# Performance work log

Hardware: AMD Instinct MI355X
Metric: run time of the kernel (lower is better)

The kernel has to match this reference:

```python
import jax, jax.numpy as jnp
import numpy as np

# Fixed problem sizes (match input_specs): B graphs of N points each, kNN with K neighbors.
B, N, K = 32, 2048, 20
F_IN, H, C = 3, 64, 40
BN = B * N
E = BN * K


def mlp(x, w1, b1, w2, b2):
    # PyG MLP([in, H, H]) with plain last layer: Lin -> ReLU -> Lin
    return jax.nn.relu(x @ w1 + b1) @ w2 + b2


def edge_conv(x, src, dst, w1, b1, w2, b2):
    # EdgeConv message for edge j->i: MLP(cat[x_i, x_j - x_i]); aggr='max' at target i.
    xi = x[dst]                      # [E, F]
    xj = x[src]                      # [E, F]
    msg = mlp(jnp.concatenate([xi, xj - xi], axis=-1), w1, b1, w2, b2)  # [E, H]
    out = jax.ops.segment_max(msg, dst, num_segments=x.shape[0])        # [BN, H]
    # nodes with no incoming edges: -inf -> 0 (torch_scatter max fill behavior)
    return jnp.where(jnp.isfinite(out), out, jnp.zeros((), out.dtype))


def dynamic_edge_conv(x, w1, b1, w2, b2):
    # Rebuild kNN graph from current features within each graph, then EdgeConv(max).
    xb = x.reshape(B, N, -1)                                   # [B, N, H]
    sq = jnp.sum(xb * xb, axis=-1)                             # [B, N]
    # squared euclidean distances [B, N, N]
    d = sq[:, :, None] - 2.0 * jnp.einsum('bnh,bmh->bnm', xb, xb) + sq[:, None, :]
    _, idx = jax.lax.top_k(-d, K)                              # [B, N, K] nearest (incl. self)
    xj = jax.vmap(lambda xg, ig: xg[ig])(xb, idx)              # [B, N, K, H]
    xi = jnp.broadcast_to(xb[:, :, None, :], xj.shape)         # [B, N, K, H]
    msg = mlp(jnp.concatenate([xi, xj - xi], axis=-1), w1, b1, w2, b2)  # [B, N, K, H]
    return jnp.max(msg, axis=2).reshape(BN, -1)                # exactly K msgs per node


def _lin_init(key, fan_in, fan_out):
    k1, k2 = jax.random.split(key)
    s = 1.0 / np.sqrt(fan_in)
    w = jax.random.uniform(k1, (fan_in, fan_out), jnp.float32, -s, s)
    b = jax.random.uniform(k2, (fan_out,), jnp.float32, -s, s)
    return w, b


def setup_inputs() -> dict:
    key = jax.random.key(0)
    ks = jax.random.split(key, 10)
    x = jax.random.normal(ks[0], (BN, F_IN), jnp.float32)
    edge_index = jax.random.randint(ks[1], (2, E), 0, BN, jnp.int64)
    batch = (jnp.arange(BN) // N).astype(jnp.int64)
    c1_w1, c1_b1 = _lin_init(ks[2], 2 * F_IN, H)
    c1_w2, c1_b2 = _lin_init(ks[3], H, H)
    d1_w1, d1_b1 = _lin_init(ks[4], 2 * H, H)
    d1_w2, d1_b2 = _lin_init(ks[5], H, H)
    d2_w1, d2_b1 = _lin_init(ks[6], 2 * H, H)
    d2_w2, d2_b2 = _lin_init(ks[7], H, H)
    lin_w, lin_b = _lin_init(ks[8], H, C)
    return dict(x=x, edge_index=edge_index, batch=batch,
                c1_w1=c1_w1, c1_b1=c1_b1, c1_w2=c1_w2, c1_b2=c1_b2,
                d1_w1=d1_w1, d1_b1=d1_b1, d1_w2=d1_w2, d1_b2=d1_b2,
                d2_w1=d2_w1, d2_b1=d2_b1, d2_w2=d2_w2, d2_b2=d2_b2,
                lin_w=lin_w, lin_b=lin_b)


def reference(x, edge_index, batch,
              c1_w1, c1_b1, c1_w2, c1_b2,
              d1_w1, d1_b1, d1_w2, d1_b2,
              d2_w1, d2_b1, d2_w2, d2_b2,
              lin_w, lin_b):
    # batch is assumed sorted with equal-size graphs (arange // N); kNN is done per graph.
    src, dst = edge_index[0], edge_index[1]
    h = edge_conv(x, src, dst, c1_w1, c1_b1, c1_w2, c1_b2)
    h = dynamic_edge_conv(jax.nn.elu(h), d1_w1, d1_b1, d1_w2, d1_b2)
    h = dynamic_edge_conv(jax.nn.elu(h), d2_w1, d2_b1, d2_w2, d2_b2)
    return h @ lin_w + lin_b
```

## Files before the change

kernel.cpp:

```cpp
#include <hip/hip_runtime.h>
#include <math.h>

#define Bg 32
#define Ng 2048
#define Kn 20
#define BNn (Bg*Ng)
#define En (BNn*Kn)
#define Hd 64
#define Cd 40

#define KK 24
#define CAPB 7

typedef __attribute__((ext_vector_type(8))) short bf16x8;
typedef __attribute__((ext_vector_type(4))) float f32x4;

__device__ __forceinline__ unsigned enc_f32(float f){
  unsigned u = __float_as_uint(f);
  return ((int)u < 0) ? ~u : (u | 0x80000000u);
}

__device__ __forceinline__ unsigned short bf16rne(float f){
  unsigned u = __float_as_uint(f);
  return (unsigned short)((u + 0x7FFFu + ((u >> 16) & 1u)) >> 16);
}

__global__ void prep_w_kernel(const float* __restrict__ w1c, const float* __restrict__ w1d1,
                              const float* __restrict__ w1d2,
                              float* __restrict__ wpq0, float* __restrict__ wpq1,
                              float* __restrict__ wpq2){
  int t = blockIdx.x*256 + threadIdx.x;
  if (t < 3*128){
    int d = t >> 7, l = t & 127;
    wpq0[t] = (l < 64) ? (w1c[d*64 + l] - w1c[(d+3)*64 + l]) : w1c[(d+3)*64 + (l-64)];
  }
  if (t < 64*128){
    int d = t >> 7, l = t & 127;
    wpq1[t] = (l < 64) ? (w1d1[d*64 + l] - w1d1[(d+64)*64 + l]) : w1d1[(d+64)*64 + (l-64)];
    wpq2[t] = (l < 64) ? (w1d2[d*64 + l] - w1d2[(d+64)*64 + l]) : w1d2[(d+64)*64 + (l-64)];
  }
}

__global__ void zero_kernel(int* __restrict__ p){
  p[blockIdx.x*256 + threadIdx.x] = 0;
}

__global__ void init_enc_kernel(unsigned int* __restrict__ enc){
  enc[blockIdx.x*256 + threadIdx.x] = 0x007FFFFFu;
}

template<int D>
__global__ __launch_bounds__(128) void gemm_pq_kernel(const float* __restrict__ x,
                               const float* __restrict__ w,
                               float* __restrict__ P, float* __restrict__ Q){
  __shared__ float xs[8*D];
  int l = threadIdx.x;
  int node0 = blockIdx.x*8;
  float wc[D];
  #pragma unroll
  for (int d=0; d<D; d++) wc[d] = w[d*128 + l];
  for (int i=l; i < 8*D; i += 128) xs[i] = x[(size_t)node0*D + i];
  __syncthreads();
  #pragma unroll
  for (int n=0; n<8; n++){
    float s = 0.f;
    #pragma unroll
    for (int d=0; d<D; d++) s = fmaf(xs[n*D+d], wc[d], s);
    int node = node0 + n;
    if (l < 64) P[(size_t)node*64 + l] = s;
    else        Q[(size_t)node*64 + (l-64)] = s;
  }
}

__global__ __launch_bounds__(256) void sqxb_kernel(const float* __restrict__ x,
        float* __restrict__ sq, unsigned short* __restrict__ xb){
  int t = blockIdx.x*256 + threadIdx.x;
  int node = t >> 6, l = t & 63;
  float v = x[t];
  xb[t] = bf16rne(v);
  float s = v*v;
  #pragma unroll
  for (int o=32; o; o>>=1) s += __shfl_xor(s, o, 64);
  if (l == 0) sq[node] = s;
}

__global__ __launch_bounds__(256) void decode_sqxb_kernel(const unsigned int* __restrict__ enc,
        const float* __restrict__ b2, float* __restrict__ x,
        float* __restrict__ sq, unsigned short* __restrict__ xb){
  int t = blockIdx.x*256 + threadIdx.x;
  int node = t >> 6, l = t & 63;
  unsigned int e = enc[t];
  unsigned int bits = (e & 0x80000000u) ? (e ^ 0x80000000u) : ~e;
  float f = __uint_as_float(bits);
  if (isfinite(f)) f += b2[l]; else f = 0.f;
  f = f > 0.f ? f : expm1f(f);
  x[t] = f;
  xb[t] = bf16rne(f);
  float s = f*f;
  #pragma unroll
  for (int o=32; o; o>>=1) s += __shfl_xor(s, o, 64);
  if (l == 0) sq[node] = s;
}

__global__ void count_kernel(const int* __restrict__ ei, int* __restrict__ deg){
  int e = blockIdx.x*256 + threadIdx.x;
  atomicAdd(&deg[ei[En + e]], 1);
}

__global__ __launch_bounds__(1024) void scan_kernel(const int* __restrict__ deg,
        int* __restrict__ rowptr, int* __restrict__ cursor){
  __shared__ int ps[1024];
  int t = threadIdx.x;
  int base = t*64;
  int s = 0;
  for (int k=0;k<64;k++) s += deg[base+k];
  ps[t] = s; __syncthreads();
  for (int off=1; off<1024; off<<=1){
    int v = (t>=off) ? ps[t-off] : 0;
    __syncthreads();
    ps[t] += v;
    __syncthreads();
  }
  int run = (t>0) ? ps[t-1] : 0;
  for (int k=0;k<64;k++){
    rowptr[base+k] = run; cursor[base+k] = run;
    run += deg[base+k];
  }
  if (t==1023) rowptr[BNn] = run;
}

__global__ void scatter_kernel(const int* __restrict__ ei, int* __restrict__ cursor,
                               int* __restrict__ csrc, int* __restrict__ enid){
  int e = blockIdx.x*256 + threadIdx.x;
  int s = ei[e], d = ei[En + e];
  int pos = atomicAdd(&cursor[d], 1);
  csrc[pos] = s;
  enid[pos] = d;
}

#define SWZ16(base, row, stridep2, byteoff) \
  ((unsigned short*)((char*)(base) + ((((row) << (stridep2)) + (byteoff)) ^ (((row) & 7) << 4))))

__global__ __launch_bounds__(256,3) void econv_gemm_kernel(
    const int* __restrict__ csrc, const int* __restrict__ enid,
    const float* __restrict__ P, const float* __restrict__ Q,
    const float* __restrict__ b1, const float* __restrict__ w2,
    unsigned int* __restrict__ enc){
  __shared__ __align__(16) char smem[49152];
  unsigned short* Ah = (unsigned short*)smem;
  unsigned short* Al = (unsigned short*)(smem + 16384);
  unsigned short* Wh = (unsigned short*)(smem + 32768);
  unsigned short* Wl = (unsigned short*)(smem + 40960);
  float* Ct = (float*)smem;
  __shared__ int eids[256];
  int tid = threadIdx.x;
  int lane = tid & 63, w = tid >> 6;
  int e0 = ((blockIdx.x & 7)*640 + (blockIdx.x >> 3))*256;

  eids[tid] = enid[e0 + tid];
  #pragma unroll
  for (int z = 0; z < 16; z++){
    int idx = z*256 + tid;
    int k = idx >> 6, n = idx & 63;
    float f = w2[idx];
    unsigned short h = bf16rne(f);
    float fh = __uint_as_float((unsigned)h << 16);
    unsigned short l = bf16rne(f - fh);
    *SWZ16(Wh, n, 7, k*2) = h;
    *SWZ16(Wl, n, 7, k*2) = l;
  }

  #pragma unroll 1
  for (int hh = 0; hh < 2; hh++){
    int eh0 = e0 + hh*128;
    __syncthreads();
    {
      int el = tid >> 1, kh2 = (tid & 1) * 32;
      int e = eh0 + el;
      int i = eids[hh*128 + el];
      int j = csrc[e];
      const float* Pr = P + (size_t)i*Hd + kh2;
      const float* Qr = Q + (size_t)j*Hd + kh2;
      const float* Br = b1 + kh2;
      #pragma unroll
      for (int m = 0; m < 4; m++){
        float4 pa = ((const float4*)Pr)[2*m], pb = ((const float4*)Pr)[2*m+1];
        float4 qa = ((const float4*)Qr)[2*m], qb = ((const float4*)Qr)[2*m+1];
        float4 ba = ((const float4*)Br)[2*m], bbv = ((const float4*)Br)[2*m+1];
        float a[8];
        a[0]=fmaxf(pa.x+qa.x+ba.x,0.f);  a[1]=fmaxf(pa.y+qa.y+ba.y,0.f);
        a[2]=fmaxf(pa.z+qa.z+ba.z,0.f);  a[3]=fmaxf(pa.w+qa.w+ba.w,0.f);
        a[4]=fmaxf(pb.x+qb.x+bbv.x,0.f); a[5]=fmaxf(pb.y+qb.y+bbv.y,0.f);
        a[6]=fmaxf(pb.z+qb.z+bbv.z,0.f); a[7]=fmaxf(pb.w+qb.w+bbv.w,0.f);
        unsigned hw[4], lw[4];
        #pragma unroll
        for (int t=0;t<4;t++){
          unsigned short h0 = bf16rne(a[2*t]);
          unsigned short h1 = bf16rne(a[2*t+1]);
          float f0 = __uint_as_float((unsigned)h0 << 16);
          float f1 = __uint_as_float((unsigned)h1 << 16);
          unsigned short l0 = bf16rne(a[2*t] - f0);
          unsigned short l1 = bf16rne(a[2*t+1] - f1);
          hw[t] = (unsigned)h0 | ((unsigned)h1 << 16);
          lw[t] = (unsigned)l0 | ((unsigned)l1 << 16);
        }
        uint4 hv = {hw[0], hw[1], hw[2], hw[3]};
        uint4 lv = {lw[0], lw[1], lw[2], lw[3]};
        *(uint4*)SWZ16(Ah, el, 7, (kh2 + 8*m)*2) = hv;
        *(uint4*)SWZ16(Al, el, 7, (kh2 + 8*m)*2) = lv;
      }
    }
    __syncthreads();
    bf16x8 Af[2][2], Lf[2][2];
    #pragma unroll
    for (int mt=0; mt<2; mt++)
      #pragma unroll
      for (int s=0; s<2; s++){
        int row = w*32 + mt*16 + (lane & 15);
        Af[mt][s] = *(const bf16x8*)SWZ16(Ah, row, 7, (s*32 + (lane>>4)*8)*2);
        Lf[mt][s] = *(const bf16x8*)SWZ16(Al, row, 7, (s*32 + (lane>>4)*8)*2);
      }
    f32x4 acc[2][4];
    #pragma unroll
    for (int mt=0; mt<2; mt++)
      #pragma unroll
      for (int nt=0; nt<4; nt++)
        acc[mt][nt] = (f32x4){0.f,0.f,0.f,0.f};
    #pragma unroll
    for (int nt=0; nt<4; nt++){
      int n = nt*16 + (lane & 15);
      bf16x8 Bh0 = *(const bf16x8*)SWZ16(Wh, n, 7, ((lane>>4)*8)*2);
      bf16x8 Bh1 = *(const bf16x8*)SWZ16(Wh, n, 7, (32 + (lane>>4)*8)*2);
      bf16x8 Bl0 = *(const bf16x8*)SWZ16(Wl, n, 7, ((lane>>4)*8)*2);
      bf16x8 Bl1 = *(const bf16x8*)SWZ16(Wl, n, 7, (32 + (lane>>4)*8)*2);
      #pragma unroll
      for (int mt=0; mt<2; mt++){
        f32x4 a_ = acc[mt][nt];
        a_ = __builtin_amdgcn_mfma_f32_16x16x32_bf16(Af[mt][0], Bh0, a_, 0, 0, 0);
        a_ = __builtin_amdgcn_mfma_f32_16x16x32_bf16(Af[mt][1], Bh1, a_, 0, 0, 0);
        a_ = __builtin_amdgcn_mfma_f32_16x16x32_bf16(Af[mt][0], Bl0, a_, 0, 0, 0);
        a_ = __builtin_amdgcn_mfma_f32_16x16x32_bf16(Af[mt][1], Bl1, a_, 0, 0, 0);
        a_ = __builtin_amdgcn_mfma_f32_16x16x32_bf16(Lf[mt][0], Bh0, a_, 0, 0, 0);
        a_ = __builtin_amdgcn_mfma_f32_16x16x32_bf16(Lf[mt][1], Bh1, a_, 0, 0, 0);
        acc[mt][nt] = a_;
      }
    }
    __syncthreads();
    #pragma unroll
    for (int mt=0; mt<2; mt++){
      int rb = w*32 + mt*16 + (lane>>4)*4;
      #pragma unroll
      for (int nt=0; nt<4; nt++){
        int ch = nt*16 + (lane & 15);
        #pragma unroll
        for (int v=0; v<4; v++)
          Ct[ch*128 + ((rb+v) ^ (ch & 31))] = acc[mt][nt][v];
      }
    }
    __syncthreads();
    {
      int ch = tid & 63, part = tid >> 6;
      int rbase = part*32;
      int cur = eids[hh*128 + rbase];
      float vmax = -INFINITY;
      #pragma unroll 1
      for (int r = 0; r < 32; r++){
        int row = rbase + r;
        int id = eids[hh*128 + row];
        float v = Ct[ch*128 + (row ^ (ch & 31))];
        if (id != cur){
          atomicMax(&enc[(size_t)cur*Hd + ch], enc_f32(vmax));
          vmax = -INFINITY; cur = id;
        }
        vmax = fmaxf(vmax, v);
      }
      atomicMax(&enc[(size_t)cur*Hd + ch], enc_f32(vmax));
    }
  }
}

__device__ __forceinline__ void ins24(unsigned (&kb)[KK], unsigned key){
  #pragma unroll
  for (int p=KK-1; p>0; p--){
    unsigned ins = (key < kb[p]) ? key : kb[p];
    kb[p] = (key < kb[p-1]) ? kb[p-1] : ins;
  }
  kb[0] = (key < kb[0]) ? key : kb[0];
}

#define KNN_FLUSH() do { \
  _Pragma("unroll 1") \
  for (int c=0;c<CAPB;c++){ \
    if (!__any(c < cnt)) break; \
    unsigned kf = (c < cnt) ? kc[c][tid] : 0xFFFFFFFFu; \
    ins24(kb, kf); \
  } \
  cnt = 0; kbLast = kb[KK-1]; \
} while(0)

#define KNN_TRY(key) do { unsigned kk_ = (key); \
  if (kk_ < kbLast){ kc[cnt][tid] = kk_; cnt++; } } while(0)

__global__ __launch_bounds__(256,4) void knn_kernel(
    const unsigned short* __restrict__ xb, const float* __restrict__ sq,
    unsigned short* __restrict__ cand){
  __shared__ __align__(16) unsigned short xjb[128*64];
  __shared__ __align__(16) unsigned short Dt[64*128];
  __shared__ unsigned kc[CAPB][256];
  __shared__ float sqs[128];

  int tid = threadIdx.x;
  int lane = tid & 63, w = tid >> 6;
  int bid = ((blockIdx.x & 7) << 7) | (blockIdx.x >> 3);
  int g  = bid >> 5;
  int r0 = (bid & 31) * 64;
  const unsigned short* xbg = xb + (size_t)g*Ng*Hd;
  const float* sg = sq + (size_t)g*Ng;

  int q = w;
  int prow = lane;
  int rw = w*16;

  bf16x8 A0, A1;
  {
    int arow = r0 + rw + (lane & 15);
    A0 = *(const bf16x8*)(xbg + (size_t)arow*Hd +      (lane>>4)*8);
    A1 = *(const bf16x8*)(xbg + (size_t)arow*Hd + 32 + (lane>>4)*8);
  }
  {
    int jr = tid >> 1, half = tid & 1;
    int jloc = (jr >> 5)*512 + (jr & 31);
    const uint4* src = (const uint4*)(xbg + (size_t)jloc*Hd + half*32);
    uint4 a = src[0], b = src[1], c2 = src[2], d2 = src[3];
    *(uint4*)SWZ16(xjb, jr, 7, half*64 +  0) = a;
    *(uint4*)SWZ16(xjb, jr, 7, half*64 + 16) = b;
    *(uint4*)SWZ16(xjb, jr, 7, half*64 + 32) = c2;
    *(uint4*)SWZ16(xjb, jr, 7, half*64 + 48) = d2;
    if (tid < 128) sqs[tid] = sg[(tid>>5)*512 + (tid&31)];
  }

  unsigned kb[KK];
  #pragma unroll
  for (int t=0;t<KK;t++) kb[t] = 0xFFFFFFFFu;
  unsigned kbLast = 0xFFFFFFFFu;
  int cnt = 0;

  __syncthreads();

  #pragma unroll 1
  for (int it = 0; it < 16; it++){
    uint4 pf0, pf1, pf2, pf3; float psq = 0.f;
    int itn = it + 1;
    int jr = tid >> 1, half = tid & 1;
    if (itn < 16){
      int jloc = (jr >> 5)*512 + itn*32 + (jr & 31);
      const uint4* src = (const uint4*)(xbg + (size_t)jloc*Hd + half*32);
      pf0 = src[0]; pf1 = src[1]; pf2 = src[2]; pf3 = src[3];
      if (tid < 128) psq = sg[(tid>>5)*512 + itn*32 + (tid&31)];
    }
    #pragma unroll
    for (int jb = 0; jb < 8; jb++){
      int brow = jb*16 + (lane & 15);
      bf16x8 B0 = *(const bf16x8*)SWZ16(xjb, brow, 7,      (lane>>4)*16);
      bf16x8 B1 = *(const bf16x8*)SWZ16(xjb, brow, 7, 64 + (lane>>4)*16);
      f32x4 acc = {0.f, 0.f, 0.f, 0.f};
      acc = __builtin_amdgcn_mfma_f32_16x16x32_bf16(A0, B0, acc, 0, 0, 0);
      acc = __builtin_amdgcn_mfma_f32_16x16x32_bf16(A1, B1, acc, 0, 0, 0);
      int col = jb*16 + (lane & 15);
      float sqv = sqs[col];
      int rbase = rw + (lane>>4)*4;
      #pragma unroll
      for (int v=0; v<4; v++){
        float f = fmaf(acc[v], -2.f, sqv);
        unsigned u = __float_as_uint(f);
        unsigned t2 = ((unsigned)((int)u >> 31)) | 0x8000u;
        *SWZ16(Dt, rbase + v, 8, col*2) = (unsigned short)((u >> 16) ^ t2);
      }
    }
    __syncthreads();
    if (it == 0){
      unsigned key[32];
      const char* dbase = (const char*)Dt + (prow << 8);
      unsigned m = (prow & 7) << 4;
      #pragma unroll
      for (int r4=0; r4<4; r4++){
        uint4 dv = *(const uint4*)(dbase + ((unsigned)(q*64 + r4*16) ^ m));
        int cb = q*512 + r4*8;
        key[r4*8+0] = (dv.x << 16) + (unsigned)(cb + 0);
        key[r4*8+1] = (dv.x & 0xFFFF0000u) | (unsigned)(cb + 1);
        key[r4*8+2] = (dv.y << 16) + (unsigned)(cb + 2);
        key[r4*8+3] = (dv.y & 0xFFFF0000u) | (unsigned)(cb + 3);
        key[r4*8+4] = (dv.z << 16) + (unsigned)(cb + 4);
        key[r4*8+5] = (dv.z & 0xFFFF0000u) | (unsigned)(cb + 5);
        key[r4*8+6] = (dv.w << 16) + (unsigned)(cb + 6);
        key[r4*8+7] = (dv.w & 0xFFFF0000u) | (unsigned)(cb + 7);
      }
      #pragma unroll
      for (int k2 = 2; k2 <= 32; k2 <<= 1){
        #pragma unroll
        for (int j2 = k2>>1; j2 > 0; j2 >>= 1){
          #pragma unroll
          for (int i2 = 0; i2 < 32; i2++){
            int ixj = i2 ^ j2;
            if (ixj > i2){
              unsigned a = key[i2], b = key[ixj];
              unsigned lo = a < b ? a : b;
              unsigned hi = a < b ? b : a;
              bool up = ((i2 & k2) == 0);
              key[i2]  = up ? lo : hi;
              key[ixj] = up ? hi : lo;
            }
          }
        }
      }
      #pragma unroll
      for (int t=0;t<KK;t++) kb[t] = key[t];
      kbLast = kb[KK-1];
    } else {
      int jbase0 = q*512 + it*32;
      const char* dbase = (const char*)Dt + (prow << 8);
      unsigned m = (prow & 7) << 4;
      #pragma unroll
      for (int r4=0; r4<4; r4++){
        uint4 dv = *(const uint4*)(dbase + ((unsigned)(q*64 + r4*16) ^ m));
        int cb = jbase0 + r4*8;
        KNN_TRY((dv.x << 16) + (unsigned)(cb + 0));
        KNN_TRY((dv.x & 0xFFFF0000u) | (unsigned)(cb + 1));
        KNN_TRY((dv.y << 16) + (unsigned)(cb + 2));
        KNN_TRY((dv.y & 0xFFFF0000u) | (unsigned)(cb + 3));
        if (__any(cnt >= 4)) KNN_FLUSH();
        KNN_TRY((dv.z << 16) + (unsigned)(cb + 4));
        KNN_TRY((dv.z & 0xFFFF0000u) | (unsigned)(cb + 5));
        KNN_TRY((dv.w << 16) + (unsigned)(cb + 6));
        KNN_TRY((dv.w & 0xFFFF0000u) | (unsigned)(cb + 7));
        if (__any(cnt >= 4)) KNN_FLUSH();
      }
    }
    if (itn < 16){
      *(uint4*)SWZ16(xjb, jr, 7, half*64 +  0) = pf0;
      *(uint4*)SWZ16(xjb, jr, 7, half*64 + 16) = pf1;
      *(uint4*)SWZ16(xjb, jr, 7, half*64 + 32) = pf2;
      *(uint4*)SWZ16(xjb, jr, 7, half*64 + 48) = pf3;
      if (tid < 128) sqs[tid] = psq;
    }
    __syncthreads();
  }
  KNN_FLUSH();
  size_t base = (size_t)(g*Ng + r0 + prow)*96 + q*24;
  #pragma unroll
  for (int t=0;t<KK;t++)
    cand[base + t] = (unsigned short)(kb[t] & 2047u);
}

__global__ __launch_bounds__(256,2) void rerank_kernel(const float* __restrict__ x,
        const unsigned short* __restrict__ cand, int* __restrict__ idx){
  __shared__ __align__(16) unsigned long long ks[4][96];
  int tid = threadIdx.x;
  int lane = tid & 63, w = tid >> 6;
  int bid = ((blockIdx.x & 7) << 11) | (blockIdx.x >> 3);
  int row = bid*4 + w;
  int g = row >> 11;
  const float* xg = x + (size_t)g*Ng*Hd;
  int chunk = lane & 3;
  int cg = lane >> 2;
  const float* xr = x + (size_t)row*Hd;
  float4 xc[4];
  #pragma unroll
  for (int it2=0; it2<4; it2++) xc[it2] = *(const float4*)(xr + 16*it2 + 4*chunk);

  int js[6];
  #pragma unroll
  for (int p=0; p<6; p++) js[p] = cand[(size_t)row*96 + p*16 + cg];

  float4 bb[6][4];
  #pragma unroll
  for (int p=0; p<6; p++){
    const float* xj = xg + (size_t)js[p]*Hd;
    #pragma unroll
    for (int it2=0; it2<4; it2++) bb[p][it2] = *(const float4*)(xj + 16*it2 + 4*chunk);
  }
  #pragma unroll
  for (int p=0; p<6; p++){
    float dot = 0.f, sqj = 0.f;
    #pragma unroll
    for (int it2=0; it2<4; it2++){
      float4 b = bb[p][it2];
      float4 a = xc[it2];
      dot = fmaf(a.x, b.x, dot); dot = fmaf(a.y, b.y, dot);
      dot = fmaf(a.z, b.z, dot); dot = fmaf(a.w, b.w, dot);
      sqj = fmaf(b.x, b.x, sqj); sqj = fmaf(b.y, b.y, sqj);
      sqj = fmaf(b.z, b.z, sqj); sqj = fmaf(b.w, b.w, sqj);
    }
    dot += __shfl_xor(dot, 1, 64); dot += __shfl_xor(dot, 2, 64);
    sqj += __shfl_xor(sqj, 1, 64); sqj += __shfl_xor(sqj, 2, 64);
    if (chunk == 0){
      float dist = fmaf(dot, -2.f, sqj);
      ks[w][p*16 + cg] = ((unsigned long long)enc_f32(dist) << 32) | (unsigned)js[p];
    }
  }
  __syncthreads();
  unsigned long long k0 = ks[w][lane];
  unsigned long long k1 = (lane < 32) ? ks[w][64 + lane] : ~0ULL;
  int r0 = 0, r1 = 0;
  #pragma unroll
  for (int c=0;c<96;c+=2){
    unsigned long long a = ks[w][c], b = ks[w][c+1];
    r0 += (a < k0) + (b < k0);
    r1 += (a < k1) + (b < k1);
  }
  if (r0 < Kn) idx[(size_t)row*Kn + r0] = g*Ng + (int)(k0 & 2047ULL);
  if (lane < 32 && r1 < Kn) idx[(size_t)row*Kn + r1] = g*Ng + (int)(k1 & 2047ULL);
}

__global__ __launch_bounds__(256,3) void emsg_kernel(
    const int* __restrict__ srcl,
    const float* __restrict__ P, const float* __restrict__ Q,
    const float* __restrict__ b1, const float* __restrict__ w2,
    unsigned int* __restrict__ enc){
  __shared__ __align__(16) char smem[49152];
  unsigned short* Ah = (unsigned short*)smem;
  unsigned short* Al = (unsigned short*)(smem + 16384);
  unsigned short* Wh = (unsigned short*)(smem + 32768);
  unsigned short* Wl = (unsigned short*)(smem + 40960);
  float* p0 = (float*)smem;
  float* p1 = (float*)(smem + 8448);
  int tid = threadIdx.x;
  int lane = tid & 63, w = tid >> 6;
  int e0 = ((blockIdx.x & 7)*640 + (blockIdx.x >> 3))*256;

  #pragma unroll
  for (int z = 0; z < 16; z++){
    int idx = z*256 + tid;
    int k = idx >> 6, n = idx & 63;
    float f = w2[idx];
    unsigned short h = bf16rne(f);
    float fh = __uint_as_float((unsigned)h << 16);
    unsigned short l = bf16rne(f - fh);
    *SWZ16(Wh, n, 7, k*2) = h;
    *SWZ16(Wl, n, 7, k*2) = l;
  }

  #pragma unroll 1
  for (int hh = 0; hh < 2; hh++){
    int eh0 = e0 + hh*128;
    __syncthreads();
    {
      int el = tid >> 1, kh = (tid & 1) * 32;
      int e = eh0 + el;
      int i = e / Kn;
      int j = srcl[e];
      const float* Pr = P + (size_t)i*Hd + kh;
      const float* Qr = Q + (size_t)j*Hd + kh;
      const float* Br = b1 + kh;
      #pragma unroll
      for (int m = 0; m < 4; m++){
        float4 pa = ((const float4*)Pr)[2*m], pb = ((const float4*)Pr)[2*m+1];
        float4 qa = ((const float4*)Qr)[2*m], qb = ((const float4*)Qr)[2*m+1];
        float4 ba = ((const float4*)Br)[2*m], bbv = ((const float4*)Br)[2*m+1];
        float a[8];
        a[0]=fmaxf(pa.x+qa.x+ba.x,0.f);  a[1]=fmaxf(pa.y+qa.y+ba.y,0.f);
        a[2]=fmaxf(pa.z+qa.z+ba.z,0.f);  a[3]=fmaxf(pa.w+qa.w+ba.w,0.f);
        a[4]=fmaxf(pb.x+qb.x+bbv.x,0.f); a[5]=fmaxf(pb.y+qb.y+bbv.y,0.f);
        a[6]=fmaxf(pb.z+qb.z+bbv.z,0.f); a[7]=fmaxf(pb.w+qb.w+bbv.w,0.f);
        unsigned hw[4], lw[4];
        #pragma unroll
        for (int t=0;t<4;t++){
          unsigned short h0 = bf16rne(a[2*t]);
          unsigned short h1 = bf16rne(a[2*t+1]);
          float f0 = __uint_as_float((unsigned)h0 << 16);
          float f1 = __uint_as_float((unsigned)h1 << 16);
          unsigned short l0 = bf16rne(a[2*t] - f0);
          unsigned short l1 = bf16rne(a[2*t+1] - f1);
          hw[t] = (unsigned)h0 | ((unsigned)h1 << 16);
          lw[t] = (unsigned)l0 | ((unsigned)l1 << 16);
        }
        uint4 hv = {hw[0], hw[1], hw[2], hw[3]};
        uint4 lv = {lw[0], lw[1], lw[2], lw[3]};
        *(uint4*)SWZ16(Ah, el, 7, (kh + 8*m)*2) = hv;
        *(uint4*)SWZ16(Al, el, 7, (kh + 8*m)*2) = lv;
      }
    }
    __syncthreads();
    bf16x8 Af[2][2], Lf[2][2];
    #pragma unroll
    for (int mt=0; mt<2; mt++)
      #pragma unroll
      for (int s=0; s<2; s++){
        int row = w*32 + mt*16 + (lane & 15);
        Af[mt][s] = *(const bf16x8*)SWZ16(Ah, row, 7, (s*32 + (lane>>4)*8)*2);
        Lf[mt][s] = *(const bf16x8*)SWZ16(Al, row, 7, (s*32 + (lane>>4)*8)*2);
      }
    f32x4 acc[2][4];
    #pragma unroll
    for (int mt=0; mt<2; mt++)
      #pragma unroll
      for (int nt=0; nt<4; nt++)
        acc[mt][nt] = (f32x4){0.f,0.f,0.f,0.f};
    #pragma unroll
    for (int nt=0; nt<4; nt++){
      int n = nt*16 + (lane & 15);
      bf16x8 Bh0 = *(const bf16x8*)SWZ16(Wh, n, 7, ((lane>>4)*8)*2);
      bf16x8 Bh1 = *(const bf16x8*)SWZ16(Wh, n, 7, (32 + (lane>>4)*8)*2);
      bf16x8 Bl0 = *(const bf16x8*)SWZ16(Wl, n, 7, ((lane>>4)*8)*2);
      bf16x8 Bl1 = *(const bf16x8*)SWZ16(Wl, n, 7, (32 + (lane>>4)*8)*2);
      #pragma unroll
      for (int mt=0; mt<2; mt++){
        f32x4 a_ = acc[mt][nt];
        a_ = __builtin_amdgcn_mfma_f32_16x16x32_bf16(Af[mt][0], Bh0, a_, 0, 0, 0);
        a_ = __builtin_amdgcn_mfma_f32_16x16x32_bf16(Af[mt][1], Bh1, a_, 0, 0, 0);
        a_ = __builtin_amdgcn_mfma_f32_16x16x32_bf16(Af[mt][0], Bl0, a_, 0, 0, 0);
        a_ = __builtin_amdgcn_mfma_f32_16x16x32_bf16(Af[mt][1], Bl1, a_, 0, 0, 0);
        a_ = __builtin_amdgcn_mfma_f32_16x16x32_bf16(Lf[mt][0], Bh0, a_, 0, 0, 0);
        a_ = __builtin_amdgcn_mfma_f32_16x16x32_bf16(Lf[mt][1], Bh1, a_, 0, 0, 0);
        acc[mt][nt] = a_;
      }
    }
    __syncthreads();
    #pragma unroll
    for (int mt=0; mt<2; mt++){
      int rb = w*32 + mt*16 + (lane>>4)*4;
      int rbg = eh0 + rb;
      int nd0 = rbg / Kn;
      int split = (nd0+1)*Kn - rbg; if (split > 4) split = 4;
      int cm = rb >> 2;
      #pragma unroll
      for (int nt=0; nt<4; nt++){
        int ch = nt*16 + (lane & 15);
        float s0v = -INFINITY, s1v = -INFINITY;
        #pragma unroll
        for (int v=0; v<4; v++){
          float val = acc[mt][nt][v];
          if (v < split) s0v = fmaxf(s0v, val); else s1v = fmaxf(s1v, val);
        }
        p0[ch*33 + cm] = s0v;
        p1[ch*33 + cm] = s1v;
      }
    }
    __syncthreads();
    int nfirst = eh0 / Kn;
    int ncnt = (eh0 + 127) / Kn - nfirst + 1;
    int ch = tid & 63;
    for (int ln = tid >> 6; ln < ncnt; ln += 4){
      int nd = nfirst + ln;
      int glo = nd*Kn;      if (glo < eh0)     glo = eh0;
      int ghi = nd*Kn + Kn; if (ghi > eh0+128) ghi = eh0+128;
      int mlo = (glo - eh0) >> 2, mhi = (ghi - 1 - eh0) >> 2;
      float v = -INFINITY;
      for (int mm = mlo; mm <= mhi; mm++){
        int bn = (eh0 + 4*mm) / Kn;
        if (bn == nd)     v = fmaxf(v, p0[ch*33 + mm]);
        if (bn + 1 == nd) v = fmaxf(v, p1[ch*33 + mm]);
      }
      atomicMax(&enc[(size_t)nd*Hd + ch], enc_f32(v));
    }
  }
}

__global__ __launch_bounds__(256) void decode_kernel(const unsigned int* __restrict__ enc,
         const float* __restrict__ b2, float* __restrict__ x){
  int t = blockIdx.x*256 + threadIdx.x;
  unsigned int e = enc[t];
  unsigned int bits = (e & 0x80000000u) ? (e ^ 0x80000000u) : ~e;
  float f = __uint_as_float(bits);
  if (isfinite(f)) f += b2[t & 63]; else f = 0.f;
  x[t] = f;
}

__global__ __launch_bounds__(64) void final_kernel(const float* __restrict__ h,
        const float* __restrict__ w, const float* __restrict__ bias,
        float* __restrict__ out){
  __shared__ float xs[Hd];
  int c = threadIdx.x;
  float wc[Hd];
  float bc = 0.f;
  if (c < Cd){
    #pragma unroll
    for (int d=0; d<Hd; d++) wc[d] = w[d*Cd + c];
    bc = bias[c];
  }
  for (int i = blockIdx.x; i < BNn; i += gridDim.x){
    __syncthreads();
    xs[c] = h[(size_t)i*Hd + c];
    __syncthreads();
    if (c < Cd){
      float s = bc;
      #pragma unroll
      for (int d=0; d<Hd; d++) s = fmaf(xs[d], wc[d], s);
      out[(size_t)i*Cd + c] = s;
    }
  }
}

extern "C" void kernel_launch(void* const* d_in, const int* in_sizes, int n_in,
                              void* d_out, int out_size, void* d_ws, size_t ws_size,
                              hipStream_t stream){
  const float* x0   = (const float*)d_in[0];
  const int*   ei   = (const int*)d_in[1];
  const float* c1w1 = (const float*)d_in[3];
  const float* c1b1 = (const float*)d_in[4];
  const float* c1w2 = (const float*)d_in[5];
  const float* c1b2 = (const float*)d_in[6];
  const float* d1w1 = (const float*)d_in[7];
  const float* d1b1 = (const float*)d_in[8];
  const float* d1w2 = (const float*)d_in[9];
  const float* d1b2 = (const float*)d_in[10];
  const float* d2w1 = (const float*)d_in[11];
  const float* d2b1 = (const float*)d_in[12];
  const float* d2w2 = (const float*)d_in[13];
  const float* d2b2 = (const float*)d_in[14];
  const float* linw = (const float*)d_in[15];
  const float* linb = (const float*)d_in[16];
  float* out = (float*)d_out;

  char* ws = (char*)d_ws;
  size_t off = 0;
  auto alloc = [&](size_t bytes)->char*{
    char* p = ws + off; off += (bytes + 255) & ~(size_t)255; return p;
  };
  float*        X    = (float*)alloc(sizeof(float)*(size_t)BNn*Hd);
  float*        P    = (float*)alloc(sizeof(float)*(size_t)BNn*Hd);
  float*        Q    = (float*)alloc(sizeof(float)*(size_t)BNn*Hd);
  float*        H2   = (float*)alloc(sizeof(float)*(size_t)BNn*Hd);
  unsigned int* ENC  = (unsigned int*)alloc(sizeof(unsigned)*(size_t)BNn*Hd);
  int*          SHRD = (int*)alloc(sizeof(int)*(size_t)En);
  int*          DEG  = (int*)alloc(sizeof(int)*BNn);
  int*          RPTR = (int*)alloc(sizeof(int)*(BNn+1));
  int*          CUR  = (int*)alloc(sizeof(int)*BNn);
  float*        SQ   = (float*)alloc(sizeof(float)*BNn);
  float*        WPQ0 = (float*)alloc(sizeof(float)*3*128);
  float*        WPQ1 = (float*)alloc(sizeof(float)*64*128);
  float*        WPQ2 = (float*)alloc(sizeof(float)*64*128);
  int*            CSRC = SHRD;
  int*            IDX  = SHRD;
  int*            ENID = (int*)H2;
  unsigned short* XB   = (unsigned short*)H2;
  unsigned short* CAND = (unsigned short*)ENC;
  (void)ws_size; (void)in_sizes; (void)n_in; (void)out_size;

  prep_w_kernel<<<32, 256, 0, stream>>>(c1w1, d1w1, d2w1, WPQ0, WPQ1, WPQ2);
  zero_kernel<<<BNn/256, 256, 0, stream>>>(DEG);
  count_kernel<<<En/256, 256, 0, stream>>>(ei, DEG);
  gemm_pq_kernel<3><<<BNn/8, 128, 0, stream>>>(x0, WPQ0, P, Q);
  scan_kernel<<<1, 1024, 0, stream>>>(DEG, RPTR, CUR);
  scatter_kernel<<<En/256, 256, 0, stream>>>(ei, CUR, CSRC, ENID);
  init_enc_kernel<<<BNn*Hd/256, 256, 0, stream>>>(ENC);
  econv_gemm_kernel<<<En/256, 256, 0, stream>>>(CSRC, ENID, P, Q, c1b1, c1w2, ENC);
  decode_sqxb_kernel<<<BNn*Hd/256, 256, 0, stream>>>(ENC, c1b2, X, SQ, XB);

  gemm_pq_kernel<64><<<BNn/8, 128, 0, stream>>>(X, WPQ1, P, Q);
  knn_kernel<<<Bg*32, 256, 0, stream>>>(XB, SQ, CAND);
  rerank_kernel<<<BNn/4, 256, 0, stream>>>(X, CAND, IDX);
  init_enc_kernel<<<BNn*Hd/256, 256, 0, stream>>>(ENC);
  emsg_kernel<<<En/256, 256, 0, stream>>>(IDX, P, Q, d1b1, d1w2, ENC);
  decode_sqxb_kernel<<<BNn*Hd/256, 256, 0, stream>>>(ENC, d1b2, X, SQ, XB);

  gemm_pq_kernel<64><<<BNn/8, 128, 0, stream>>>(X, WPQ2, P, Q);
  knn_kernel<<<Bg*32, 256, 0, stream>>>(XB, SQ, CAND);
  rerank_kernel<<<BNn/4, 256, 0, stream>>>(X, CAND, IDX);
  init_enc_kernel<<<BNn*Hd/256, 256, 0, stream>>>(ENC);
  emsg_kernel<<<En/256, 256, 0, stream>>>(IDX, P, Q, d2b1, d2w2, ENC);
  decode_kernel<<<BNn*Hd/256, 256, 0, stream>>>(ENC, d2b2, H2);

  final_kernel<<<8192, 64, 0, stream>>>(H2, linw, linb, out);
}
```

Baseline: 1.333 ms.

## Replace serial top-k insertion flush with bitonic sort-and-merge network

The kNN candidate flush used to insert buffered keys one at a time into the sorted 24-entry list, each insertion a full compare-shift pass. It now sorts up to 8 buffered candidates with a bitonic network and merges them with the 24 current best through a 32-wide bitonic merge, keeping the lowest 24. The flush fires after every 8 candidates whenever any lane has a pending entry, and the buffer capacity grows to 8. This trades the serial per-key insertion for a fixed-cost network, but the merge runs even when a lane holds only a single candidate, and it uses more registers.

Result: no change. 1.309 ms (-1.8%).

```diff
diff --git a/kernel.cpp b/kernel.cpp
--- a/kernel.cpp
+++ b/kernel.cpp
@@ -10,7 +10,7 @@
 #define Cd 40
 
 #define KK 24
-#define CAPB 7
+#define CAPB 8
 
 typedef __attribute__((ext_vector_type(8))) short bf16x8;
 typedef __attribute__((ext_vector_type(4))) float f32x4;
@@ -279,22 +279,41 @@
   }
 }
 
-__device__ __forceinline__ void ins24(unsigned (&kb)[KK], unsigned key){
-  #pragma unroll
-  for (int p=KK-1; p>0; p--){
-    unsigned ins = (key < kb[p]) ? key : kb[p];
-    kb[p] = (key < kb[p-1]) ? kb[p-1] : ins;
-  }
-  kb[0] = (key < kb[0]) ? key : kb[0];
-}
-
-#define KNN_FLUSH() do { \
-  _Pragma("unroll 1") \
-  for (int c=0;c<CAPB;c++){ \
-    if (!__any(c < cnt)) break; \
-    unsigned kf = (c < cnt) ? kc[c][tid] : 0xFFFFFFFFu; \
-    ins24(kb, kf); \
-  } \
+#define KNN_MFLUSH() do { \
+  unsigned Lm[32]; \
+  _Pragma("unroll") \
+  for (int t=0;t<KK;t++) Lm[t] = kb[t]; \
+  unsigned bm[8]; \
+  _Pragma("unroll") \
+  for (int t=0;t<8;t++) bm[t] = (t < cnt) ? kc[t][tid] : 0xFFFFFFFFu; \
+  _Pragma("unroll") \
+  for (int k2=2;k2<=8;k2<<=1) \
+    _Pragma("unroll") \
+    for (int j2=k2>>1;j2>0;j2>>=1) \
+      _Pragma("unroll") \
+      for (int i2=0;i2<8;i2++){ \
+        int ixj=i2^j2; \
+        if (ixj>i2){ \
+          unsigned a=bm[i2], c=bm[ixj]; \
+          unsigned lo = a<c?a:c, hi = a<c?c:a; \
+          bool up = ((i2 & k2)==0); \
+          bm[i2] = up?lo:hi; bm[ixj] = up?hi:lo; \
+        } \
+      } \
+  _Pragma("unroll") \
+  for (int t=0;t<8;t++) Lm[24+t] = bm[7-t]; \
+  _Pragma("unroll") \
+  for (int j2=16;j2>0;j2>>=1) \
+    _Pragma("unroll") \
+    for (int i2=0;i2<32;i2++){ \
+      int ixj=i2^j2; \
+      if (ixj>i2){ \
+        unsigned a=Lm[i2], c=Lm[ixj]; \
+        Lm[i2] = a<c?a:c; Lm[ixj] = a<c?c:a; \
+      } \
+    } \
+  _Pragma("unroll") \
+  for (int t=0;t<KK;t++) kb[t] = Lm[t]; \
   cnt = 0; kbLast = kb[KK-1]; \
 } while(0)
 
@@ -428,12 +447,11 @@
         KNN_TRY((dv.x & 0xFFFF0000u) | (unsigned)(cb + 1));
         KNN_TRY((dv.y << 16) + (unsigned)(cb + 2));
         KNN_TRY((dv.y & 0xFFFF0000u) | (unsigned)(cb + 3));
-        if (__any(cnt >= 4)) KNN_FLUSH();
         KNN_TRY((dv.z << 16) + (unsigned)(cb + 4));
         KNN_TRY((dv.z & 0xFFFF0000u) | (unsigned)(cb + 5));
         KNN_TRY((dv.w << 16) + (unsigned)(cb + 6));
         KNN_TRY((dv.w & 0xFFFF0000u) | (unsigned)(cb + 7));
-        if (__any(cnt >= 4)) KNN_FLUSH();
+        if (__any(cnt)) KNN_MFLUSH();
       }
     }
     if (itn < 16){
@@ -445,7 +463,7 @@
     }
     __syncthreads();
   }
-  KNN_FLUSH();
+  if (__any(cnt)) KNN_MFLUSH();
   size_t base = (size_t)(g*Ng + r0 + prow)*96 + q*24;
   #pragma unroll
   for (int t=0;t<KK;t++)
```
